# Optimization experiments

Hardware: AMD Instinct MI355X
Metric: run time of the kernel (lower is better)

The kernel has to match this reference:

```python
import jax, jax.numpy as jnp
import numpy as np

BN_EPS = 1e-5


def setup_inputs() -> dict:
    key = jax.random.key(0)
    ks = jax.random.split(key, 6)
    B, C, N = 4, 256, 4096
    d = C // 4
    x = jax.random.normal(ks[0], (B, C, N), dtype=jnp.float32)
    # q_conv.weight tied to k_conv.weight -> single wq used for both
    wq = jax.random.normal(ks[1], (d, C), dtype=jnp.float32) * (1.0 / np.sqrt(C))
    wv = jax.random.normal(ks[2], (C, C), dtype=jnp.float32) * (1.0 / np.sqrt(C))
    bv = jax.random.normal(ks[3], (C,), dtype=jnp.float32) * 0.01
    wt = jax.random.normal(ks[4], (C, C), dtype=jnp.float32) * (1.0 / np.sqrt(C))
    bt = jax.random.normal(ks[5], (C,), dtype=jnp.float32) * 0.01
    gamma = jnp.ones((C,), dtype=jnp.float32)
    beta = jnp.zeros((C,), dtype=jnp.float32)
    return {"x": x, "wq": wq, "wv": wv, "bv": bv, "wt": wt, "bt": bt,
            "gamma": gamma, "beta": beta}


def reference(x, wq, wv, bv, wt, bt, gamma, beta):
    # x: [B, C, N]
    # 1x1 conv projections (weight-tied Q/K)
    x_q = jnp.einsum('dc,bcn->bnd', wq, x)            # [B, N, d]
    x_k = jnp.einsum('dc,bcn->bdn', wq, x)            # [B, d, N]
    x_v = jnp.einsum('oc,bcn->bon', wv, x) + bv[None, :, None]  # [B, C, N]

    energy = jnp.einsum('bnd,bdm->bnm', x_q, x_k)     # [B, N, N]
    attn = jax.nn.softmax(energy, axis=-1)            # row softmax
    # L1 column-normalize (offset-attention double normalization)
    attn = attn / (1e-9 + jnp.sum(attn, axis=1, keepdims=True))

    x_a = jnp.einsum('bcn,bnm->bcm', x_v, attn)       # [B, C, N]
    x_d = x - x_a

    t = jnp.einsum('oc,bcn->bon', wt, x_d) + bt[None, :, None]  # trans_conv
    # BatchNorm1d in training mode: batch stats over (B, N) per channel
    mean = jnp.mean(t, axis=(0, 2), keepdims=True)
    var = jnp.var(t, axis=(0, 2), keepdims=True)
    t_hat = (t - mean) * jax.lax.rsqrt(var + BN_EPS)
    x_r = jax.nn.relu(gamma[None, :, None] * t_hat + beta[None, :, None])
    return x + x_r
```

## Files before the change

kernel.cpp:

```cpp
#include <hip/hip_runtime.h>

#define BB 4
#define CC 256
#define NN 4096
#define DD 64

typedef _Float16 h8_t __attribute__((ext_vector_type(8)));
typedef _Float16 h4_t __attribute__((ext_vector_type(4)));
typedef float fx4 __attribute__((ext_vector_type(4)));

#define MFMA16(a, b, c) __builtin_amdgcn_mfma_f32_16x16x32_f16((a), (b), (c), 0, 0, 0)

__global__ __launch_bounds__(256) void k0_prep(
    const float* __restrict__ wq, const float* __restrict__ wv, const float* __restrict__ wt,
    _Float16* __restrict__ wqH, _Float16* __restrict__ wvH, _Float16* __restrict__ wtH,
    float* __restrict__ bnsum, float* __restrict__ bnsumsq) {
  int i = blockIdx.x * 256 + threadIdx.x;
  int stride = gridDim.x * 256;
  for (int j = i; j < DD * CC; j += stride) wqH[j] = (_Float16)wq[j];
  for (int j = i; j < CC * CC; j += stride) wvH[j] = (_Float16)wv[j];
  for (int j = i; j < CC * CC; j += stride) wtH[j] = (_Float16)wt[j];
  if (i < CC) { bnsum[i] = 0.f; bnsumsq[i] = 0.f; }
}

__global__ __launch_bounds__(256) void k1a_transpose(const float* __restrict__ x,
                                                     _Float16* __restrict__ xt) {
  __shared__ float tile[32][33];
  int b = blockIdx.z;
  int c0 = blockIdx.y * 32, n0 = blockIdx.x * 32;
  int t = threadIdx.x;
  int tn = t & 31, tc = t >> 5;
  const float* xb = x + (size_t)b * CC * NN;
#pragma unroll
  for (int i = 0; i < 4; i++) {
    int c = tc + i * 8;
    tile[c][tn] = xb[(size_t)(c0 + c) * NN + n0 + tn];
  }
  __syncthreads();
  _Float16* xtb = xt + (size_t)b * NN * CC;
#pragma unroll
  for (int i = 0; i < 4; i++) {
    int n = tc + i * 8;
    xtb[(size_t)(n0 + n) * CC + c0 + tn] = (_Float16)tile[tn][n];
  }
}

__global__ __launch_bounds__(256, 2) void k1b_proj(
    const _Float16* __restrict__ xt, const _Float16* __restrict__ wqH,
    const _Float16* __restrict__ wvH, const float* __restrict__ bv,
    _Float16* __restrict__ qh, _Float16* __restrict__ vh) {
  int L = blockIdx.x;
  int xcd = L & 7, j = L >> 3;
  int b = xcd >> 1;
  int nB = ((xcd & 1) * 64 + j) * 32;
  int w = threadIdx.x >> 6, lane = threadIdx.x & 63;
  int g = lane >> 4, q = lane & 15;
  int wsub = w & 1, h = w >> 1;
  int n = nB + wsub * 16 + q;
  const _Float16* xr = xt + ((size_t)b * NN + n) * CC;
  fx4 accQ[4] = {};
  fx4 accV[8] = {};
  for (int kt = 0; kt < 8; kt++) {
    h8_t bf = *(const h8_t*)(xr + kt * 32 + g * 8);
    if (h == 0) {
#pragma unroll
      for (int ot = 0; ot < 4; ot++) {
        h8_t a = *(const h8_t*)(wqH + (size_t)(ot * 16 + q) * CC + kt * 32 + g * 8);
        accQ[ot] = MFMA16(a, bf, accQ[ot]);
      }
    }
#pragma unroll
    for (int ot = 0; ot < 8; ot++) {
      int o16 = h * 8 + ot;
      h8_t a = *(const h8_t*)(wvH + (size_t)(o16 * 16 + q) * CC + kt * 32 + g * 8);
      accV[ot] = MFMA16(a, bf, accV[ot]);
    }
  }
  if (h == 0) {
    _Float16* qr = qh + ((size_t)b * NN + n) * DD;
#pragma unroll
    for (int ot = 0; ot < 4; ot++) {
      h4_t hq;
#pragma unroll
      for (int r = 0; r < 4; r++) hq[r] = (_Float16)accQ[ot][r];
      *(h4_t*)(qr + ot * 16 + g * 4) = hq;
    }
  }
#pragma unroll
  for (int ot = 0; ot < 8; ot++) {
#pragma unroll
    for (int r = 0; r < 4; r++) {
      int o = (h * 8 + ot) * 16 + g * 4 + r;
      vh[((size_t)b * CC + o) * NN + n] = (_Float16)(accV[ot][r] + bv[o]);
    }
  }
}

__global__ __launch_bounds__(512, 4) void k2_stats(
    const _Float16* __restrict__ qh, float* __restrict__ rowmax,
    float* __restrict__ rowsuminv) {
  __shared__ float redb[8][32];
  __shared__ float rmS[32];
  int L = blockIdx.x;
  int xcd = L & 7;
  int b = xcd >> 1;
  int mi = (L & 1) * 64 + (L >> 3);
  int mB = mi * 32;
  int w = threadIdx.x >> 6, lane = threadIdx.x & 63;
  int g = lane >> 4, q = lane & 15;
  const _Float16* qb = qh + (size_t)b * NN * DD;
  h8_t aq[2][2];
#pragma unroll
  for (int mt = 0; mt < 2; mt++) {
    aq[mt][0] = *(const h8_t*)(qb + (size_t)(mB + mt * 16 + q) * DD + g * 8);
    aq[mt][1] = *(const h8_t*)(qb + (size_t)(mB + mt * 16 + q) * DD + 32 + g * 8);
  }
  fx4 rmax[2];
#pragma unroll
  for (int mt = 0; mt < 2; mt++)
#pragma unroll
    for (int r = 0; r < 4; r++) rmax[mt][r] = -1e30f;
  for (int ch = 0; ch < 32; ch++) {
    int n0 = ch * 128 + w * 16;
    h8_t b0 = *(const h8_t*)(qb + (size_t)(n0 + q) * DD + g * 8);
    h8_t b1 = *(const h8_t*)(qb + (size_t)(n0 + q) * DD + 32 + g * 8);
#pragma unroll
    for (int mt = 0; mt < 2; mt++) {
      fx4 e = {};
      e = MFMA16(aq[mt][0], b0, e);
      e = MFMA16(aq[mt][1], b1, e);
#pragma unroll
      for (int r = 0; r < 4; r++) rmax[mt][r] = fmaxf(rmax[mt][r], e[r]);
    }
  }
#pragma unroll
  for (int off = 1; off < 16; off <<= 1)
#pragma unroll
    for (int mt = 0; mt < 2; mt++)
#pragma unroll
      for (int r = 0; r < 4; r++)
        rmax[mt][r] = fmaxf(rmax[mt][r], __shfl_xor(rmax[mt][r], off));
  if (q == 0) {
#pragma unroll
    for (int mt = 0; mt < 2; mt++)
#pragma unroll
      for (int r = 0; r < 4; r++) redb[w][mt * 16 + g * 4 + r] = rmax[mt][r];
  }
  __syncthreads();
  if (threadIdx.x < 32) {
    float M = redb[0][threadIdx.x];
#pragma unroll
    for (int w2 = 1; w2 < 8; w2++) M = fmaxf(M, redb[w2][threadIdx.x]);
    rmS[threadIdx.x] = M;
    rowmax[b * NN + mB + threadIdx.x] = M;
  }
  __syncthreads();
  float rmv[2][4];
#pragma unroll
  for (int mt = 0; mt < 2; mt++)
#pragma unroll
    for (int r = 0; r < 4; r++) rmv[mt][r] = rmS[mt * 16 + g * 4 + r];
  fx4 s[2] = {};
  for (int ch = 0; ch < 32; ch++) {
    int n0 = ch * 128 + w * 16;
    h8_t b0 = *(const h8_t*)(qb + (size_t)(n0 + q) * DD + g * 8);
    h8_t b1 = *(const h8_t*)(qb + (size_t)(n0 + q) * DD + 32 + g * 8);
#pragma unroll
    for (int mt = 0; mt < 2; mt++) {
      fx4 e = {};
      e = MFMA16(aq[mt][0], b0, e);
      e = MFMA16(aq[mt][1], b1, e);
#pragma unroll
      for (int r = 0; r < 4; r++) s[mt][r] += __expf(e[r] - rmv[mt][r]);
    }
  }
#pragma unroll
  for (int off = 1; off < 16; off <<= 1)
#pragma unroll
    for (int mt = 0; mt < 2; mt++)
#pragma unroll
      for (int r = 0; r < 4; r++) s[mt][r] += __shfl_xor(s[mt][r], off);
  if (q == 0) {
#pragma unroll
    for (int mt = 0; mt < 2; mt++)
#pragma unroll
      for (int r = 0; r < 4; r++) redb[w][mt * 16 + g * 4 + r] = s[mt][r];
  }
  __syncthreads();
  if (threadIdx.x < 32) {
    float S = redb[0][threadIdx.x];
#pragma unroll
    for (int w2 = 1; w2 < 8; w2++) S += redb[w2][threadIdx.x];
    rowsuminv[b * NN + mB + threadIdx.x] = 1.f / S;
  }
}

#define PSTR 264
__global__ __launch_bounds__(512, 4) void k4_main(
    const _Float16* __restrict__ qh, const _Float16* __restrict__ vh,
    const _Float16* __restrict__ wtH, const float* __restrict__ rowmax,
    const float* __restrict__ rowsuminv, const _Float16* __restrict__ xt,
    const float* __restrict__ bt, _Float16* __restrict__ th,
    float* __restrict__ bnsum, float* __restrict__ bnsumsq) {
  __shared__ _Float16 Pb[2][32 * PSTR];
  __shared__ _Float16 xdT[32 * PSTR];
  __shared__ float csLDS[8][32];
  __shared__ float csT[32];
  int L = blockIdx.x;
  int xcd = L & 7;
  int b = xcd >> 1;
  int mi = (L & 1) * 64 + (L >> 3);
  int mB = mi * 32;
  int w = threadIdx.x >> 6, lane = threadIdx.x & 63;
  int g = lane >> 4, q = lane & 15;
  const _Float16* qb = qh + (size_t)b * NN * DD;
  const _Float16* vb = vh + (size_t)b * CC * NN;
  const float* rm = rowmax + b * NN;
  const float* ri = rowsuminv + b * NN;

  h8_t aq[2][2];
#pragma unroll
  for (int mt = 0; mt < 2; mt++) {
    aq[mt][0] = *(const h8_t*)(qb + (size_t)(mB + mt * 16 + q) * DD + g * 8);
    aq[mt][1] = *(const h8_t*)(qb + (size_t)(mB + mt * 16 + q) * DD + 32 + g * 8);
  }

  float csum[2] = {0.f, 0.f};
  h8_t pa0[2], pa1[2];

  auto loadK = [&](int ph) {
#pragma unroll
    for (int sc = 0; sc < 2; sc++) {
      int n0 = ph * 256 + sc * 128 + w * 16;
      pa0[sc] = *(const h8_t*)(qb + (size_t)(n0 + q) * DD + g * 8);
      pa1[sc] = *(const h8_t*)(qb + (size_t)(n0 + q) * DD + 32 + g * 8);
    }
  };
  auto buildP = [&](int ph, int nb) {
#pragma unroll
    for (int sc = 0; sc < 2; sc++) {
      int n0 = ph * 256 + sc * 128 + w * 16;
      fx4 rmv = *(const fx4*)(rm + n0 + 4 * g);
      fx4 riv = *(const fx4*)(ri + n0 + 4 * g);
#pragma unroll
      for (int mt = 0; mt < 2; mt++) {
        fx4 e = {};
        e = MFMA16(pa0[sc], aq[mt][0], e);
        e = MFMA16(pa1[sc], aq[mt][1], e);
        h4_t p;
        float sacc = 0.f;
#pragma unroll
        for (int r = 0; r < 4; r++) {
          float pv = __expf(e[r] - rmv[r]) * riv[r];
          p[r] = (_Float16)pv;
          sacc += pv;
        }
        csum[mt] += sacc;
        *(h4_t*)&Pb[nb][(mt * 16 + q) * PSTR + sc * 128 + w * 16 + 4 * g] = p;
      }
    }
  };

  loadK(0);
  buildP(0, 0);
  loadK(1);
  __syncthreads();

  fx4 acc[2][2] = {};
  for (int ph = 0; ph < 16; ph++) {
    int cur = ph & 1;
    const _Float16* vr0 = vb + (size_t)(32 * w + q) * NN + ph * 256;
    const _Float16* vr1 = vb + (size_t)(32 * w + 16 + q) * NN + ph * 256;
    h8_t av0[4], av1[4];
#pragma unroll
    for (int p0 = 0; p0 < 4; p0++) {
      av0[p0] = *(const h8_t*)(vr0 + p0 * 32 + g * 8);
      av1[p0] = *(const h8_t*)(vr1 + p0 * 32 + g * 8);
    }
    if (ph < 15) buildP(ph + 1, cur ^ 1);
    if (ph < 14) loadK(ph + 2);
#pragma unroll
    for (int kt = 0; kt < 8; kt++) {
      int pp = kt & 3;
      h8_t bp0 = *(const h8_t*)&Pb[cur][q * PSTR + kt * 32 + g * 8];
      h8_t bp1 = *(const h8_t*)&Pb[cur][(16 + q) * PSTR + kt * 32 + g * 8];
      acc[0][0] = MFMA16(av0[pp], bp0, acc[0][0]);
      acc[0][1] = MFMA16(av0[pp], bp1, acc[0][1]);
      acc[1][0] = MFMA16(av1[pp], bp0, acc[1][0]);
      acc[1][1] = MFMA16(av1[pp], bp1, acc[1][1]);
      if (kt < 4) {
        av0[pp] = *(const h8_t*)(vr0 + (kt + 4) * 32 + g * 8);
        av1[pp] = *(const h8_t*)(vr1 + (kt + 4) * 32 + g * 8);
      }
    }
    __syncthreads();
  }

#pragma unroll
  for (int mt = 0; mt < 2; mt++) {
    float cs = csum[mt];
    cs += __shfl_xor(cs, 16);
    cs += __shfl_xor(cs, 32);
    if (lane < 16) csLDS[w][mt * 16 + q] = cs;
  }
  __syncthreads();
  if (threadIdx.x < 32) {
    float s = 0.f;
#pragma unroll
    for (int w2 = 0; w2 < 8; w2++) s += csLDS[w2][threadIdx.x];
    csT[threadIdx.x] = 1.f / (1e-9f + s);
  }
  __syncthreads();
  float cinv[2] = {csT[q], csT[16 + q]};

#pragma unroll
  for (int ct = 0; ct < 2; ct++) {
#pragma unroll
    for (int mt = 0; mt < 2; mt++) {
      h4_t xv = *(const h4_t*)(xt + ((size_t)b * NN + mB + mt * 16 + q) * CC + 32 * w + ct * 16 + 4 * g);
      h4_t hd;
#pragma unroll
      for (int r = 0; r < 4; r++) {
        float xd = (float)xv[r] - acc[ct][mt][r] * cinv[mt];
        hd[r] = (_Float16)xd;
      }
      *(h4_t*)&xdT[(mt * 16 + q) * PSTR + 32 * w + ct * 16 + 4 * g] = hd;
    }
  }
  __syncthreads();

  fx4 acct[2][2] = {};
  for (int kt = 0; kt < 8; kt++) {
    h8_t bx0 = *(const h8_t*)&xdT[q * PSTR + kt * 32 + g * 8];
    h8_t bx1 = *(const h8_t*)&xdT[(16 + q) * PSTR + kt * 32 + g * 8];
#pragma unroll
    for (int ot = 0; ot < 2; ot++) {
      h8_t a = *(const h8_t*)(wtH + (size_t)(32 * w + ot * 16 + q) * CC + kt * 32 + g * 8);
      acct[ot][0] = MFMA16(a, bx0, acct[ot][0]);
      acct[ot][1] = MFMA16(a, bx1, acct[ot][1]);
    }
  }
#pragma unroll
  for (int ot = 0; ot < 2; ot++) {
#pragma unroll
    for (int r = 0; r < 4; r++) {
      int o = 32 * w + ot * 16 + 4 * g + r;
      float btv = bt[o];
      float t0 = acct[ot][0][r] + btv;
      float t1 = acct[ot][1][r] + btv;
      th[((size_t)b * CC + o) * NN + mB + q] = (_Float16)t0;
      th[((size_t)b * CC + o) * NN + mB + 16 + q] = (_Float16)t1;
      float s1 = t0 + t1, s2 = t0 * t0 + t1 * t1;
#pragma unroll
      for (int off = 1; off < 16; off <<= 1) {
        s1 += __shfl_xor(s1, off);
        s2 += __shfl_xor(s2, off);
      }
      if (q == 0) {
        atomicAdd(&bnsum[o], s1);
        atomicAdd(&bnsumsq[o], s2);
      }
    }
  }
}

__global__ __launch_bounds__(256) void k6_final(
    const float* __restrict__ x, const _Float16* __restrict__ th,
    const float* __restrict__ bnsum, const float* __restrict__ bnsumsq,
    const float* __restrict__ gamma, const float* __restrict__ beta,
    float* __restrict__ out) {
  size_t i = (size_t)blockIdx.x * 256 + threadIdx.x;
  size_t base = i * 8;
  int c = (int)((base >> 12) & 255);
  float inv = 1.f / (float)(BB * NN);
  float mean = bnsum[c] * inv;
  float var = bnsumsq[c] * inv - mean * mean;
  float sc = gamma[c] * rsqrtf(var + 1e-5f);
  float sh = beta[c] - mean * sc;
  h8_t t8 = *(const h8_t*)(th + base);
  fx4 x0 = *(const fx4*)(x + base);
  fx4 x1 = *(const fx4*)(x + base + 4);
  fx4 o0, o1;
#pragma unroll
  for (int j2 = 0; j2 < 4; j2++) {
    o0[j2] = x0[j2] + fmaxf(0.f, sc * (float)t8[j2] + sh);
    o1[j2] = x1[j2] + fmaxf(0.f, sc * (float)t8[j2 + 4] + sh);
  }
  *(fx4*)(out + base) = o0;
  *(fx4*)(out + base + 4) = o1;
}

extern "C" void kernel_launch(void* const* d_in, const int* in_sizes, int n_in,
                              void* d_out, int out_size, void* d_ws, size_t ws_size,
                              hipStream_t stream) {
  const float* x = (const float*)d_in[0];
  const float* wq = (const float*)d_in[1];
  const float* wv = (const float*)d_in[2];
  const float* bv = (const float*)d_in[3];
  const float* wt = (const float*)d_in[4];
  const float* bt = (const float*)d_in[5];
  const float* gamma = (const float*)d_in[6];
  const float* beta = (const float*)d_in[7];
  char* ws = (char*)d_ws;
  _Float16* qh = (_Float16*)(ws + 0);
  _Float16* vh = (_Float16*)(ws + 2097152);
  _Float16* xt = (_Float16*)(ws + 10485760);
  _Float16* wqH = (_Float16*)(ws + 18874368);
  _Float16* wvH = (_Float16*)(ws + 18907136);
  _Float16* wtH = (_Float16*)(ws + 19038208);
  float* rowmax = (float*)(ws + 19169280);
  float* rowsuminv = (float*)(ws + 19234816);
  float* bnsum = (float*)(ws + 19365888);
  float* bnsumsq = (float*)(ws + 19366912);
  _Float16* th = (_Float16*)(ws + 19369984);

  hipLaunchKernelGGL(k0_prep, dim3(64), dim3(256), 0, stream,
                     wq, wv, wt, wqH, wvH, wtH, bnsum, bnsumsq);
  hipLaunchKernelGGL(k1a_transpose, dim3(128, 8, 4), dim3(256), 0, stream, x, xt);
  hipLaunchKernelGGL(k1b_proj, dim3(512), dim3(256), 0, stream, xt, wqH, wvH, bv, qh, vh);
  hipLaunchKernelGGL(k2_stats, dim3(512), dim3(512), 0, stream, qh, rowmax, rowsuminv);
  hipLaunchKernelGGL(k4_main, dim3(512), dim3(512), 0, stream, qh, vh, wtH,
                     rowmax, rowsuminv, xt, bt, th, bnsum, bnsumsq);
  hipLaunchKernelGGL(k6_final, dim3(2048), dim3(256), 0, stream,
                     x, th, bnsum, bnsumsq, gamma, beta, (float*)d_out);
}
```

Before: 376.1 us.

## Materialize attention matrix to HBM and split fused attention into P, PV, trans kernels

Replaces the fused k4_main, which recomputed P in LDS per tile, with three kernels. k3_pmat writes the full normalized P^T matrix (B x N x N fp16) to global memory with an XOR swizzle and accumulates column sums atomically. k4_pv runs a tiled V·P GEMM using global_load_lds async staging with double buffering. k5_trans does the trans_conv GEMM plus the BN statistics. This trades P recompute and low MFMA reuse for a large extra HBM round-trip of about 128 MB written and read back.

Result: no change. 370.4 us (-1.5%).

```diff
diff --git a/kernel.cpp b/kernel.cpp
--- a/kernel.cpp
+++ b/kernel.cpp
@@ -11,16 +11,22 @@
 
 #define MFMA16(a, b, c) __builtin_amdgcn_mfma_f32_16x16x32_f16((a), (b), (c), 0, 0, 0)
 
+#define GLOAD16(g, l)                                                          \
+  __builtin_amdgcn_global_load_lds(                                            \
+      (const __attribute__((address_space(1))) unsigned int*)(g),              \
+      (__attribute__((address_space(3))) unsigned int*)(l), 16, 0, 0)
+
 __global__ __launch_bounds__(256) void k0_prep(
     const float* __restrict__ wq, const float* __restrict__ wv, const float* __restrict__ wt,
     _Float16* __restrict__ wqH, _Float16* __restrict__ wvH, _Float16* __restrict__ wtH,
-    float* __restrict__ bnsum, float* __restrict__ bnsumsq) {
+    float* __restrict__ bnsum, float* __restrict__ bnsumsq, float* __restrict__ colsum) {
   int i = blockIdx.x * 256 + threadIdx.x;
   int stride = gridDim.x * 256;
   for (int j = i; j < DD * CC; j += stride) wqH[j] = (_Float16)wq[j];
   for (int j = i; j < CC * CC; j += stride) wvH[j] = (_Float16)wv[j];
   for (int j = i; j < CC * CC; j += stride) wtH[j] = (_Float16)wt[j];
   if (i < CC) { bnsum[i] = 0.f; bnsumsq[i] = 0.f; }
+  if (i < BB * NN) colsum[i] = 0.f;
 }
 
 __global__ __launch_bounds__(256) void k1a_transpose(const float* __restrict__ x,
@@ -91,7 +97,8 @@
 #pragma unroll
     for (int r = 0; r < 4; r++) {
       int o = (h * 8 + ot) * 16 + g * 4 + r;
-      vh[((size_t)b * CC + o) * NN + n] = (_Float16)(accV[ot][r] + bv[o]);
+      int nsw = (n & ~63) | ((((n >> 3) & 7) ^ (o & 7)) << 3) | (n & 7);
+      vh[((size_t)b * CC + o) * NN + nsw] = (_Float16)(accV[ot][r] + bv[o]);
     }
   }
 }
@@ -195,162 +202,193 @@
   }
 }
 
-#define PSTR 264
-__global__ __launch_bounds__(512, 4) void k4_main(
-    const _Float16* __restrict__ qh, const _Float16* __restrict__ vh,
-    const _Float16* __restrict__ wtH, const float* __restrict__ rowmax,
-    const float* __restrict__ rowsuminv, const _Float16* __restrict__ xt,
+__global__ __launch_bounds__(512, 2) void k3_pmat(
+    const _Float16* __restrict__ qh, const float* __restrict__ rowmax,
+    const float* __restrict__ rowsuminv, _Float16* __restrict__ PT,
+    float* __restrict__ colsum) {
+  int nB = blockIdx.x * 128, mB = blockIdx.y * 128, b = blockIdx.z;
+  int w = threadIdx.x >> 6, lane = threadIdx.x & 63;
+  int g = lane >> 4, q = lane & 15;
+  int iw = w >> 2, jw = w & 3;
+  const _Float16* qb = qh + (size_t)b * NN * DD;
+  const float* rm = rowmax + b * NN;
+  const float* ri = rowsuminv + b * NN;
+  h8_t af[4][2], bf[2][2];
+#pragma unroll
+  for (int it = 0; it < 4; it++) {
+    int nr = nB + iw * 64 + it * 16 + q;
+#pragma unroll
+    for (int kt = 0; kt < 2; kt++)
+      af[it][kt] = *(const h8_t*)(qb + (size_t)nr * DD + kt * 32 + g * 8);
+  }
+#pragma unroll
+  for (int jt = 0; jt < 2; jt++) {
+    int mr = mB + jw * 32 + jt * 16 + q;
+#pragma unroll
+    for (int kt = 0; kt < 2; kt++)
+      bf[jt][kt] = *(const h8_t*)(qb + (size_t)mr * DD + kt * 32 + g * 8);
+  }
+  float cs[2] = {0.f, 0.f};
+#pragma unroll
+  for (int it = 0; it < 4; it++) {
+    int n4 = nB + iw * 64 + it * 16 + 4 * g;
+    fx4 rmv = *(const fx4*)(rm + n4);
+    fx4 riv = *(const fx4*)(ri + n4);
+#pragma unroll
+    for (int jt = 0; jt < 2; jt++) {
+      fx4 e = {};
+      e = MFMA16(af[it][0], bf[jt][0], e);
+      e = MFMA16(af[it][1], bf[jt][1], e);
+      int m = mB + jw * 32 + jt * 16 + q;
+      h4_t p;
+      float sacc = 0.f;
+#pragma unroll
+      for (int r = 0; r < 4; r++) {
+        float pv = __expf(e[r] - rmv[r]) * riv[r];
+        p[r] = (_Float16)pv;
+        sacc += pv;
+      }
+      cs[jt] += sacc;
+      int nsw = (n4 & ~63) | ((((n4 >> 3) & 7) ^ (m & 7)) << 3) | (n4 & 7);
+      *(h4_t*)&PT[((size_t)b * NN + m) * NN + nsw] = p;
+    }
+  }
+#pragma unroll
+  for (int jt = 0; jt < 2; jt++) {
+    float s = cs[jt];
+    s += __shfl_xor(s, 16);
+    s += __shfl_xor(s, 32);
+    if (lane < 16)
+      atomicAdd(&colsum[b * NN + mB + jw * 32 + jt * 16 + q], s);
+  }
+}
+
+__global__ __launch_bounds__(256, 2) void k4_pv(
+    const _Float16* __restrict__ vh, const _Float16* __restrict__ PT,
+    const float* __restrict__ colsum, const float* __restrict__ x,
+    _Float16* __restrict__ xdT) {
+  __shared__ _Float16 Vt[2][128 * 64];
+  __shared__ _Float16 Pt[2][64 * 64];
+  int c0 = blockIdx.x * 128, m0 = blockIdx.y * 64, b = blockIdx.z;
+  int w = threadIdx.x >> 6, lane = threadIdx.x & 63;
+  int g = lane >> 4, q = lane & 15;
+  int cw = w >> 1, mw = w & 1;
+  const _Float16* vb = vh + (size_t)b * CC * NN;
+  const _Float16* pb = PT + (size_t)b * NN * NN;
+  int lrow = lane >> 3, lcol = (lane & 7) * 8;
+
+  auto stage = [&](int buf, int k) {
+    int n0 = k * 64;
+#pragma unroll
+    for (int j = 0; j < 6; j++) {
+      int blk = j * 4 + w;
+      if (blk < 16) {
+        int row = blk * 8 + lrow;
+        GLOAD16(vb + (size_t)(c0 + row) * NN + n0 + lcol,
+                (char*)&Vt[buf][0] + blk * 1024);
+      } else {
+        int row = (blk - 16) * 8 + lrow;
+        GLOAD16(pb + (size_t)(m0 + row) * NN + n0 + lcol,
+                (char*)&Pt[buf][0] + (blk - 16) * 1024);
+      }
+    }
+  };
+
+  stage(0, 0);
+  __syncthreads();
+  fx4 acc[4][2] = {};
+  int swz = (q & 7) << 4;
+  int cur = 0;
+  for (int k = 0; k < 64; k++) {
+    if (k < 63) stage(cur ^ 1, k + 1);
+    const char* Vb = (const char*)&Vt[cur][0];
+    const char* Pb2 = (const char*)&Pt[cur][0];
+#pragma unroll
+    for (int kt = 0; kt < 2; kt++) {
+      int kb = ((kt * 4 + g) << 4) ^ swz;
+      h8_t a[4], bb[2];
+#pragma unroll
+      for (int ct = 0; ct < 4; ct++)
+        a[ct] = *(const h8_t*)(Vb + ((cw * 64 + ct * 16 + q) << 7) + kb);
+#pragma unroll
+      for (int mt = 0; mt < 2; mt++)
+        bb[mt] = *(const h8_t*)(Pb2 + ((mw * 32 + mt * 16 + q) << 7) + kb);
+#pragma unroll
+      for (int ct = 0; ct < 4; ct++)
+#pragma unroll
+        for (int mt = 0; mt < 2; mt++)
+          acc[ct][mt] = MFMA16(a[ct], bb[mt], acc[ct][mt]);
+    }
+    __syncthreads();
+    cur ^= 1;
+  }
+
+  float cinv[2];
+#pragma unroll
+  for (int mt = 0; mt < 2; mt++)
+    cinv[mt] = 1.f / (1e-9f + colsum[b * NN + m0 + mw * 32 + mt * 16 + q]);
+  const float* xb = x + (size_t)b * CC * NN;
+#pragma unroll
+  for (int ct = 0; ct < 4; ct++) {
+#pragma unroll
+    for (int mt = 0; mt < 2; mt++) {
+      int m = m0 + mw * 32 + mt * 16 + q;
+      int cb = c0 + cw * 64 + ct * 16 + 4 * g;
+      h4_t hd;
+#pragma unroll
+      for (int r = 0; r < 4; r++) {
+        float xv = xb[(size_t)(cb + r) * NN + m];
+        hd[r] = (_Float16)(xv - acc[ct][mt][r] * cinv[mt]);
+      }
+      *(h4_t*)&xdT[((size_t)b * NN + m) * CC + cb] = hd;
+    }
+  }
+}
+
+__global__ __launch_bounds__(256, 2) void k5_trans(
+    const _Float16* __restrict__ xdT, const _Float16* __restrict__ wtH,
     const float* __restrict__ bt, _Float16* __restrict__ th,
     float* __restrict__ bnsum, float* __restrict__ bnsumsq) {
-  __shared__ _Float16 Pb[2][32 * PSTR];
-  __shared__ _Float16 xdT[32 * PSTR];
-  __shared__ float csLDS[8][32];
-  __shared__ float csT[32];
-  int L = blockIdx.x;
-  int xcd = L & 7;
-  int b = xcd >> 1;
-  int mi = (L & 1) * 64 + (L >> 3);
-  int mB = mi * 32;
-  int w = threadIdx.x >> 6, lane = threadIdx.x & 63;
-  int g = lane >> 4, q = lane & 15;
-  const _Float16* qb = qh + (size_t)b * NN * DD;
-  const _Float16* vb = vh + (size_t)b * CC * NN;
-  const float* rm = rowmax + b * NN;
-  const float* ri = rowsuminv + b * NN;
-
-  h8_t aq[2][2];
-#pragma unroll
-  for (int mt = 0; mt < 2; mt++) {
-    aq[mt][0] = *(const h8_t*)(qb + (size_t)(mB + mt * 16 + q) * DD + g * 8);
-    aq[mt][1] = *(const h8_t*)(qb + (size_t)(mB + mt * 16 + q) * DD + 32 + g * 8);
-  }
-
-  float csum[2] = {0.f, 0.f};
-  h8_t pa0[2], pa1[2];
-
-  auto loadK = [&](int ph) {
-#pragma unroll
-    for (int sc = 0; sc < 2; sc++) {
-      int n0 = ph * 256 + sc * 128 + w * 16;
-      pa0[sc] = *(const h8_t*)(qb + (size_t)(n0 + q) * DD + g * 8);
-      pa1[sc] = *(const h8_t*)(qb + (size_t)(n0 + q) * DD + 32 + g * 8);
-    }
-  };
-  auto buildP = [&](int ph, int nb) {
-#pragma unroll
-    for (int sc = 0; sc < 2; sc++) {
-      int n0 = ph * 256 + sc * 128 + w * 16;
-      fx4 rmv = *(const fx4*)(rm + n0 + 4 * g);
-      fx4 riv = *(const fx4*)(ri + n0 + 4 * g);
-#pragma unroll
-      for (int mt = 0; mt < 2; mt++) {
-        fx4 e = {};
-        e = MFMA16(pa0[sc], aq[mt][0], e);
-        e = MFMA16(pa1[sc], aq[mt][1], e);
-        h4_t p;
-        float sacc = 0.f;
-#pragma unroll
-        for (int r = 0; r < 4; r++) {
-          float pv = __expf(e[r] - rmv[r]) * riv[r];
-          p[r] = (_Float16)pv;
-          sacc += pv;
-        }
-        csum[mt] += sacc;
-        *(h4_t*)&Pb[nb][(mt * 16 + q) * PSTR + sc * 128 + w * 16 + 4 * g] = p;
-      }
-    }
-  };
-
-  loadK(0);
-  buildP(0, 0);
-  loadK(1);
-  __syncthreads();
-
-  fx4 acc[2][2] = {};
-  for (int ph = 0; ph < 16; ph++) {
-    int cur = ph & 1;
-    const _Float16* vr0 = vb + (size_t)(32 * w + q) * NN + ph * 256;
-    const _Float16* vr1 = vb + (size_t)(32 * w + 16 + q) * NN + ph * 256;
-    h8_t av0[4], av1[4];
-#pragma unroll
-    for (int p0 = 0; p0 < 4; p0++) {
-      av0[p0] = *(const h8_t*)(vr0 + p0 * 32 + g * 8);
-      av1[p0] = *(const h8_t*)(vr1 + p0 * 32 + g * 8);
-    }
-    if (ph < 15) buildP(ph + 1, cur ^ 1);
-    if (ph < 14) loadK(ph + 2);
-#pragma unroll
-    for (int kt = 0; kt < 8; kt++) {
-      int pp = kt & 3;
-      h8_t bp0 = *(const h8_t*)&Pb[cur][q * PSTR + kt * 32 + g * 8];
-      h8_t bp1 = *(const h8_t*)&Pb[cur][(16 + q) * PSTR + kt * 32 + g * 8];
-      acc[0][0] = MFMA16(av0[pp], bp0, acc[0][0]);
-      acc[0][1] = MFMA16(av0[pp], bp1, acc[0][1]);
-      acc[1][0] = MFMA16(av1[pp], bp0, acc[1][0]);
-      acc[1][1] = MFMA16(av1[pp], bp1, acc[1][1]);
-      if (kt < 4) {
-        av0[pp] = *(const h8_t*)(vr0 + (kt + 4) * 32 + g * 8);
-        av1[pp] = *(const h8_t*)(vr1 + (kt + 4) * 32 + g * 8);
-      }
-    }
-    __syncthreads();
-  }
-
-#pragma unroll
-  for (int mt = 0; mt < 2; mt++) {
-    float cs = csum[mt];
-    cs += __shfl_xor(cs, 16);
-    cs += __shfl_xor(cs, 32);
-    if (lane < 16) csLDS[w][mt * 16 + q] = cs;
-  }
-  __syncthreads();
-  if (threadIdx.x < 32) {
-    float s = 0.f;
-#pragma unroll
-    for (int w2 = 0; w2 < 8; w2++) s += csLDS[w2][threadIdx.x];
-    csT[threadIdx.x] = 1.f / (1e-9f + s);
-  }
-  __syncthreads();
-  float cinv[2] = {csT[q], csT[16 + q]};
-
-#pragma unroll
-  for (int ct = 0; ct < 2; ct++) {
-#pragma unroll
-    for (int mt = 0; mt < 2; mt++) {
-      h4_t xv = *(const h4_t*)(xt + ((size_t)b * NN + mB + mt * 16 + q) * CC + 32 * w + ct * 16 + 4 * g);
-      h4_t hd;
-#pragma unroll
-      for (int r = 0; r < 4; r++) {
-        float xd = (float)xv[r] - acc[ct][mt][r] * cinv[mt];
-        hd[r] = (_Float16)xd;
-      }
-      *(h4_t*)&xdT[(mt * 16 + q) * PSTR + 32 * w + ct * 16 + 4 * g] = hd;
-    }
-  }
-  __syncthreads();
-
-  fx4 acct[2][2] = {};
+  __shared__ _Float16 xl[64 * 264];
+  int m0 = blockIdx.x * 64, b = blockIdx.y;
+  int t = threadIdx.x;
+  int w = t >> 6, lane = t & 63, g = lane >> 4, q = lane & 15;
+  {
+    int row = t >> 2, cb = (t & 3) * 64;
+    const _Float16* src = xdT + ((size_t)b * NN + m0 + row) * CC + cb;
+#pragma unroll
+    for (int j = 0; j < 8; j++)
+      *(h8_t*)&xl[row * 264 + cb + j * 8] = *(const h8_t*)(src + j * 8);
+  }
+  __syncthreads();
+  fx4 acc[4][4] = {};
   for (int kt = 0; kt < 8; kt++) {
-    h8_t bx0 = *(const h8_t*)&xdT[q * PSTR + kt * 32 + g * 8];
-    h8_t bx1 = *(const h8_t*)&xdT[(16 + q) * PSTR + kt * 32 + g * 8];
-#pragma unroll
-    for (int ot = 0; ot < 2; ot++) {
-      h8_t a = *(const h8_t*)(wtH + (size_t)(32 * w + ot * 16 + q) * CC + kt * 32 + g * 8);
-      acct[ot][0] = MFMA16(a, bx0, acct[ot][0]);
-      acct[ot][1] = MFMA16(a, bx1, acct[ot][1]);
-    }
-  }
-#pragma unroll
-  for (int ot = 0; ot < 2; ot++) {
+    h8_t bx[4];
+#pragma unroll
+    for (int mt = 0; mt < 4; mt++)
+      bx[mt] = *(const h8_t*)&xl[(mt * 16 + q) * 264 + kt * 32 + g * 8];
+#pragma unroll
+    for (int ot = 0; ot < 4; ot++) {
+      h8_t a = *(const h8_t*)(wtH + (size_t)(w * 64 + ot * 16 + q) * CC + kt * 32 + g * 8);
+#pragma unroll
+      for (int mt = 0; mt < 4; mt++)
+        acc[ot][mt] = MFMA16(a, bx[mt], acc[ot][mt]);
+    }
+  }
+#pragma unroll
+  for (int ot = 0; ot < 4; ot++) {
 #pragma unroll
     for (int r = 0; r < 4; r++) {
-      int o = 32 * w + ot * 16 + 4 * g + r;
+      int o = w * 64 + ot * 16 + 4 * g + r;
       float btv = bt[o];
-      float t0 = acct[ot][0][r] + btv;
-      float t1 = acct[ot][1][r] + btv;
-      th[((size_t)b * CC + o) * NN + mB + q] = (_Float16)t0;
-      th[((size_t)b * CC + o) * NN + mB + 16 + q] = (_Float16)t1;
-      float s1 = t0 + t1, s2 = t0 * t0 + t1 * t1;
+      float s1 = 0.f, s2 = 0.f;
+#pragma unroll
+      for (int mt = 0; mt < 4; mt++) {
+        float tv = acc[ot][mt][r] + btv;
+        th[((size_t)b * CC + o) * NN + m0 + mt * 16 + q] = (_Float16)tv;
+        s1 += tv;
+        s2 += tv * tv;
+      }
 #pragma unroll
       for (int off = 1; off < 16; off <<= 1) {
         s1 += __shfl_xor(s1, off);
@@ -402,25 +440,32 @@
   const float* gamma = (const float*)d_in[6];
   const float* beta = (const float*)d_in[7];
   char* ws = (char*)d_ws;
-  _Float16* qh = (_Float16*)(ws + 0);
-  _Float16* vh = (_Float16*)(ws + 2097152);
-  _Float16* xt = (_Float16*)(ws + 10485760);
-  _Float16* wqH = (_Float16*)(ws + 18874368);
-  _Float16* wvH = (_Float16*)(ws + 18907136);
-  _Float16* wtH = (_Float16*)(ws + 19038208);
-  float* rowmax = (float*)(ws + 19169280);
-  float* rowsuminv = (float*)(ws + 19234816);
-  float* bnsum = (float*)(ws + 19365888);
-  float* bnsumsq = (float*)(ws + 19366912);
-  _Float16* th = (_Float16*)(ws + 19369984);
+  _Float16* PT = (_Float16*)(ws + 0);
+  _Float16* qh = (_Float16*)(ws + 134217728);
+  _Float16* vh = (_Float16*)(ws + 136314880);
+  _Float16* xt = (_Float16*)(ws + 144703488);
+  _Float16* xdT = (_Float16*)(ws + 153092096);
+  _Float16* th = (_Float16*)(ws + 161480704);
+  _Float16* wqH = (_Float16*)(ws + 169869312);
+  _Float16* wvH = (_Float16*)(ws + 169902080);
+  _Float16* wtH = (_Float16*)(ws + 170033152);
+  float* rowmax = (float*)(ws + 170164224);
+  float* rowsuminv = (float*)(ws + 170229760);
+  float* colsum = (float*)(ws + 170295296);
+  float* bnsum = (float*)(ws + 170360832);
+  float* bnsumsq = (float*)(ws + 170361856);
 
   hipLaunchKernelGGL(k0_prep, dim3(64), dim3(256), 0, stream,
-                     wq, wv, wt, wqH, wvH, wtH, bnsum, bnsumsq);
+                     wq, wv, wt, wqH, wvH, wtH, bnsum, bnsumsq, colsum);
   hipLaunchKernelGGL(k1a_transpose, dim3(128, 8, 4), dim3(256), 0, stream, x, xt);
   hipLaunchKernelGGL(k1b_proj, dim3(512), dim3(256), 0, stream, xt, wqH, wvH, bv, qh, vh);
   hipLaunchKernelGGL(k2_stats, dim3(512), dim3(512), 0, stream, qh, rowmax, rowsuminv);
-  hipLaunchKernelGGL(k4_main, dim3(512), dim3(512), 0, stream, qh, vh, wtH,
-                     rowmax, rowsuminv, xt, bt, th, bnsum, bnsumsq);
+  hipLaunchKernelGGL(k3_pmat, dim3(32, 32, 4), dim3(512), 0, stream,
+                     qh, rowmax, rowsuminv, PT, colsum);
+  hipLaunchKernelGGL(k4_pv, dim3(2, 64, 4), dim3(256), 0, stream,
+                     vh, PT, colsum, x, xdT);
+  hipLaunchKernelGGL(k5_trans, dim3(64, 4), dim3(256), 0, stream,
+                     xdT, wtH, bt, th, bnsum, bnsumsq);
   hipLaunchKernelGGL(k6_final, dim3(2048), dim3(256), 0, stream,
                      x, th, bnsum, bnsumsq, gamma, beta, (float*)d_out);
 }
```
